# Kernel tuning notes

Measured on AMD Instinct MI355X. Metric: run time of the kernel, lower is better.

## Reference

```python
import jax, jax.numpy as jnp
import numpy as np

B, S, H = 4, 256, 768
E, R, D = 200, 200, 25
NUM_ENT_TYPES, NUM_REL_TYPES = 9, 5
MAX_ENT_LEN = 100


def _make_span_mask(key, b, n, s, max_len):
    k1, k2 = jax.random.split(key)
    start = jax.random.randint(k1, (b, n), 0, s - max_len)
    length = jax.random.randint(k2, (b, n), 1, max_len)
    pos = jnp.arange(s)[None, None, :]
    return ((pos >= start[..., None]) & (pos < (start + length)[..., None])).astype(jnp.int32)


def setup_inputs() -> dict:
    key = jax.random.key(0)
    ks = jax.random.split(key, 9)
    lhs = jax.random.normal(ks[0], (B, S, H), dtype=jnp.float32)
    entity_mask = _make_span_mask(ks[1], B, E, S, 30)          # [B,E,S], span length < MAX_ENT_LEN
    relations = jax.random.randint(ks[2], (B, R, 2), 0, E).astype(jnp.int32)
    relation_context_mask = _make_span_mask(ks[3], B, R, S, 30)  # [B,R,S]
    size_emb = jax.random.normal(ks[4], (MAX_ENT_LEN, D), dtype=jnp.float32) * 0.02
    span_w = jax.random.normal(ks[5], (NUM_ENT_TYPES, D + 2 * H), dtype=jnp.float32) * 0.02
    span_b = jax.random.normal(ks[6], (NUM_ENT_TYPES,), dtype=jnp.float32) * 0.02
    rel_w = jax.random.normal(ks[7], (NUM_REL_TYPES, 2 * D + 3 * H), dtype=jnp.float32) * 0.02
    rel_b = jax.random.normal(ks[8], (NUM_REL_TYPES,), dtype=jnp.float32) * 0.02
    return {"last_hidden_state": lhs, "entity_mask": entity_mask, "relations": relations,
            "relation_context_mask": relation_context_mask, "size_emb": size_emb,
            "span_w": span_w, "span_b": span_b, "rel_w": rel_w, "rel_b": rel_b}


def _masked_maxpool(lhs, mask):
    # lhs: [B,S,H], mask: [B,N,S] (0/1) -> [B,N,H]
    # Faithful to torch: broadcast multiply (zeros included in max), then max over S.
    masked = lhs[:, None, :, :] * mask[:, :, :, None].astype(lhs.dtype)  # [B,N,S,H]
    return masked.max(axis=2)


def reference(last_hidden_state, entity_mask, relations, relation_context_mask,
              size_emb, span_w, span_b, rel_w, rel_b):
    b = last_hidden_state.shape[0]
    # --- entity classification ---
    entity_size = size_emb[entity_mask.sum(axis=-1)]               # [B,E,D]
    entity = _masked_maxpool(last_hidden_state, entity_mask)       # [B,E,H]
    context = last_hidden_state[:, 0, :]                           # CLS pooling [B,H]
    ctx = jnp.broadcast_to(context[:, None, :], entity.shape)      # [B,E,H]
    entity_repr = jnp.concatenate([entity, ctx, entity_size], axis=-1)
    entity_logit = entity_repr @ span_w.T + span_b                 # [B,E,num_entity_types]
    # --- relation classification ---
    rel_ctx = _masked_maxpool(last_hidden_state, relation_context_mask)  # [B,R,H]
    bidx = jnp.arange(b)[:, None, None]
    pair = entity[bidx, relations]                                 # [B,R,2,H]
    pair = pair.reshape(b, relations.shape[1], -1)                 # [B,R,2H]
    pair_size = entity_size[bidx, relations].reshape(b, relations.shape[1], -1)  # [B,R,2D]
    relation_repr = jnp.concatenate([rel_ctx, pair, pair_size], axis=-1)
    relation_logit = relation_repr @ rel_w.T + rel_b               # [B,R,num_relation_types]
    return entity_logit, relation_logit
```

## Files before the change

### kernel.cpp

```cpp
#include <hip/hip_runtime.h>
#include <math.h>

#define Bb 4
#define Ss 256
#define Hh 768
#define Ee 200
#define Rr 200
#define Dd 25
#define NET 9
#define NRT 5
#define ENT_REPR (Dd + 2*Hh)
#define REL_REPR (2*Dd + 3*Hh)
#define TPB 192
#define H4 (Hh/4)
#define NCG 48
#define NLVL 4


__device__ __forceinline__ float4 max4(float4 a, float4 b) {
    return make_float4(fmaxf(a.x, b.x), fmaxf(a.y, b.y),
                       fmaxf(a.z, b.z), fmaxf(a.w, b.w));
}

__global__ __launch_bounds__(256) void rmq_build(
    const float4* __restrict__ lhs4, float4* __restrict__ rmq4)
{
    const int b   = blockIdx.x / NCG;
    const int cg  = blockIdx.x % NCG;
    const int cf0 = cg * 4;
    const int s   = threadIdx.x;

    __shared__ float4 bufA[Ss][5];
    __shared__ float4 bufB[Ss][5];

    const float4* src = lhs4 + ((size_t)b * Ss + s) * H4 + cf0;
    #pragma unroll
    for (int j = 0; j < 4; ++j) bufA[s][j] = src[j];
    __syncthreads();

    float4 (*A)[5] = bufA;
    float4 (*Bf)[5] = bufB;
    #pragma unroll
    for (int l = 1; l <= NLVL; ++l) {
        const int sp = min(s + (1 << (l - 1)), Ss - 1);
        #pragma unroll
        for (int j = 0; j < 4; ++j)
            Bf[s][j] = max4(A[s][j], A[sp][j]);
        __syncthreads();
        float4* lvl = rmq4 + ((size_t)(l - 1) * Bb + b) * Ss * H4 + cf0;
        #pragma unroll
        for (int p = 0; p < 4; ++p) {
            const int sr = (s >> 2) + (p << 6);
            const int j  = s & 3;
            lvl[(size_t)sr * H4 + j] = Bf[sr][j];
        }
        float4 (*t)[5] = A; A = Bf; Bf = t;
        __syncthreads();
    }
}

__device__ __forceinline__ void span_decode(const unsigned long long* bal,
                                            int& first, int& length)
{
    const unsigned long long b0 = bal[0], b1 = bal[1], b2 = bal[2], b3 = bal[3];
    length = __popcll(b0) + __popcll(b1) + __popcll(b2) + __popcll(b3);
    if (b0)      first = __ffsll(b0) - 1;
    else if (b1) first = 63  + __ffsll(b1);
    else if (b2) first = 127 + __ffsll(b2);
    else         first = 191 + __ffsll(b3);
}

__device__ __forceinline__ float4 rmq_query(
    const float4* __restrict__ lhs4, const float4* __restrict__ rmq4,
    int b, int first, int length, int tid)
{
    const int l  = 31 - __clz(length);
    const int i2 = first + length - (1 << l);
    const float4* base = (l == 0)
        ? (lhs4 + (size_t)b * Ss * H4)
        : (rmq4 + ((size_t)(l - 1) * Bb + b) * Ss * H4);
    const float4 t1 = base[(size_t)first * H4 + tid];
    const float4 t2 = base[(size_t)i2    * H4 + tid];
    float4 m = max4(t1, t2);
    return max4(m, make_float4(0.f, 0.f, 0.f, 0.f));
}

__global__ __launch_bounds__(TPB) void spert_fused(
    const float4* __restrict__ lhs4,
    const float4* __restrict__ rmq4,
    const int*   __restrict__ ent_mask,
    const int*   __restrict__ relations,
    const int*   __restrict__ rel_mask,
    const float* __restrict__ size_emb,
    const float* __restrict__ span_w,
    const float* __restrict__ span_b,
    const float* __restrict__ rel_w,
    const float* __restrict__ rel_b,
    float* __restrict__ ent_logit,
    float* __restrict__ rel_logit)
{
    const int tid  = threadIdx.x;
    const int wave = tid >> 6;
    const int lane = tid & 63;

    __shared__ unsigned long long s_bal[3][4];
    __shared__ float s_part[3][NET];

    if (blockIdx.x < Bb * Ee) {
        const int b = blockIdx.x / Ee;
        const int e = blockIdx.x % Ee;

        const int* mrow = ent_mask + (size_t)(b*Ee + e)*Ss;
        {
            const unsigned long long bal = __ballot(mrow[tid] != 0);
            if (lane == 0) s_bal[0][wave] = bal;
        }
        if (tid < 64) {
            const unsigned long long bal = __ballot(mrow[192 + tid] != 0);
            if (tid == 0) s_bal[0][3] = bal;
        }
        __syncthreads();

        int first, length;
        span_decode(s_bal[0], first, length);

        const float4 v  = rmq_query(lhs4, rmq4, b, first, length, tid);
        const float4 cx = lhs4[(size_t)b * Ss * H4 + tid];
        const float  sz = (tid < Dd) ? size_emb[length * Dd + tid] : 0.0f;

        float sums[NET];
        #pragma unroll
        for (int t = 0; t < NET; ++t) {
            const float* w  = span_w + (size_t)t * ENT_REPR;
            const float* wa = w + 4*tid;
            const float* wb = w + Hh + 4*tid;
            float s = v.x*wa[0]  + v.y*wa[1]  + v.z*wa[2]  + v.w*wa[3]
                    + cx.x*wb[0] + cx.y*wb[1] + cx.z*wb[2] + cx.w*wb[3];
            if (tid < Dd) s += sz * w[2*Hh + tid];
            sums[t] = s;
        }
        #pragma unroll
        for (int t = 0; t < NET; ++t) {
            float s = sums[t];
            #pragma unroll
            for (int o = 32; o > 0; o >>= 1) s += __shfl_xor(s, o, 64);
            if (lane == 0) s_part[wave][t] = s;
        }
        __syncthreads();
        if (tid < NET) {
            ent_logit[(size_t)(b*Ee + e)*NET + tid] =
                s_part[0][tid] + s_part[1][tid] + s_part[2][tid] + span_b[tid];
        }
    } else {
        const int idx = blockIdx.x - Bb * Ee;
        const int b = idx / Rr;
        const int r = idx % Rr;

        const int e1 = relations[(size_t)(b*Rr + r)*2 + 0];
        const int e2 = relations[(size_t)(b*Rr + r)*2 + 1];

        const int* mrc = rel_mask + (size_t)(b*Rr + r)*Ss;
        const int* mr1 = ent_mask + (size_t)(b*Ee + e1)*Ss;
        const int* mr2 = ent_mask + (size_t)(b*Ee + e2)*Ss;
        {
            const unsigned long long bc = __ballot(mrc[tid] != 0);
            const unsigned long long b1 = __ballot(mr1[tid] != 0);
            const unsigned long long b2 = __ballot(mr2[tid] != 0);
            if (lane == 0) {
                s_bal[0][wave] = bc;
                s_bal[1][wave] = b1;
                s_bal[2][wave] = b2;
            }
        }
        if (tid < 64) {
            const unsigned long long bc = __ballot(mrc[192 + tid] != 0);
            const unsigned long long b1 = __ballot(mr1[192 + tid] != 0);
            const unsigned long long b2 = __ballot(mr2[192 + tid] != 0);
            if (tid == 0) {
                s_bal[0][3] = bc;
                s_bal[1][3] = b1;
                s_bal[2][3] = b2;
            }
        }
        __syncthreads();

        int fc, nc; span_decode(s_bal[0], fc, nc);
        int f1, n1; span_decode(s_bal[1], f1, n1);
        int f2, n2; span_decode(s_bal[2], f2, n2);

        const float4 cx = rmq_query(lhs4, rmq4, b, fc, nc, tid);
        const float4 a  = rmq_query(lhs4, rmq4, b, f1, n1, tid);
        const float4 d  = rmq_query(lhs4, rmq4, b, f2, n2, tid);
        const float sz1 = (tid < Dd) ? size_emb[n1 * Dd + tid] : 0.0f;
        const float sz2 = (tid < Dd) ? size_emb[n2 * Dd + tid] : 0.0f;

        float sums[NRT];
        #pragma unroll
        for (int t = 0; t < NRT; ++t) {
            const float* w  = rel_w + (size_t)t * REL_REPR;
            const float* wc = w + 4*tid;
            const float* wa = w + Hh + 4*tid;
            const float* wd = w + 2*Hh + 4*tid;
            float s = cx.x*wc[0] + cx.y*wc[1] + cx.z*wc[2] + cx.w*wc[3]
                    + a.x*wa[0]  + a.y*wa[1]  + a.z*wa[2]  + a.w*wa[3]
                    + d.x*wd[0]  + d.y*wd[1]  + d.z*wd[2]  + d.w*wd[3];
            if (tid < Dd) s += sz1 * w[3*Hh + tid] + sz2 * w[3*Hh + Dd + tid];
            sums[t] = s;
        }
        #pragma unroll
        for (int t = 0; t < NRT; ++t) {
            float s = sums[t];
            #pragma unroll
            for (int o = 32; o > 0; o >>= 1) s += __shfl_xor(s, o, 64);
            if (lane == 0) s_part[wave][t] = s;
        }
        __syncthreads();
        if (tid < NRT) {
            rel_logit[(size_t)(b*Rr + r)*NRT + tid] =
                s_part[0][tid] + s_part[1][tid] + s_part[2][tid] + rel_b[tid];
        }
    }
}

extern "C" void kernel_launch(void* const* d_in, const int* in_sizes, int n_in,
                              void* d_out, int out_size, void* d_ws, size_t ws_size,
                              hipStream_t stream) {
    const float* lhs       = (const float*)d_in[0];
    const int*   ent_mask  = (const int*)  d_in[1];
    const int*   relations = (const int*)  d_in[2];
    const int*   rel_mask  = (const int*)  d_in[3];
    const float* size_emb  = (const float*)d_in[4];
    const float* span_w    = (const float*)d_in[5];
    const float* span_b    = (const float*)d_in[6];
    const float* rel_w     = (const float*)d_in[7];
    const float* rel_b     = (const float*)d_in[8];

    float* ent_logit = (float*)d_out;
    float* rel_logit = (float*)d_out + (size_t)Bb*Ee*NET;

    const float4* lhs4 = (const float4*)lhs;
    float4*       rmq4 = (float4*)d_ws;

    rmq_build<<<Bb * NCG, 256, 0, stream>>>(lhs4, rmq4);

    spert_fused<<<Bb*Ee + Bb*Rr, TPB, 0, stream>>>(
        lhs4, rmq4, ent_mask, relations, rel_mask, size_emb,
        span_w, span_b, rel_w, rel_b, ent_logit, rel_logit);
}
```

Before: 85.60 us.

## Map each span/relation to one wavefront and pad weights for float4 loads

Changes the main kernel so each wavefront handles one entity or relation instead of a 192-thread block. Span bounds are decoded with int4 mask loads and wave shuffles, which removes shared memory and block barriers. The weights are copied into a padded workspace in the build kernel so the dot products can use aligned float4 loads. Each lane now does three times the work, and the padding copy adds a small amount of extra work to the build step.

```diff
diff --git a/kernel.cpp b/kernel.cpp
--- a/kernel.cpp
+++ b/kernel.cpp
@@ -9,216 +9,197 @@
 #define Dd 25
 #define NET 9
 #define NRT 5
-#define ENT_REPR (Dd + 2*Hh)
-#define REL_REPR (2*Dd + 3*Hh)
-#define TPB 192
 #define H4 (Hh/4)
 #define NCG 48
 #define NLVL 4
+#define SPAD 1568
+#define RPAD 2368
+#define RMQ_F (4u * Bb * Ss * Hh)
 
 
 __device__ __forceinline__ float4 max4(float4 a, float4 b) {
     return make_float4(fmaxf(a.x, b.x), fmaxf(a.y, b.y),
                        fmaxf(a.z, b.z), fmaxf(a.w, b.w));
 }
-
-__global__ __launch_bounds__(256) void rmq_build(
-    const float4* __restrict__ lhs4, float4* __restrict__ rmq4)
-{
-    const int b   = blockIdx.x / NCG;
-    const int cg  = blockIdx.x % NCG;
-    const int cf0 = cg * 4;
-    const int s   = threadIdx.x;
-
-    __shared__ float4 bufA[Ss][5];
-    __shared__ float4 bufB[Ss][5];
-
-    const float4* src = lhs4 + ((size_t)b * Ss + s) * H4 + cf0;
+__device__ __forceinline__ float dot4(float4 a, float4 b) {
+    return a.x*b.x + a.y*b.y + a.z*b.z + a.w*b.w;
+}
+
+__global__ __launch_bounds__(256) void build_kernel(
+    const float4* __restrict__ lhs4,
+    const float* __restrict__ span_w, const float* __restrict__ rel_w,
+    float4* __restrict__ rmq4,
+    float* __restrict__ span_wp, float* __restrict__ rel_wp)
+{
+    if (blockIdx.x < Bb * NCG) {
+        const int b   = blockIdx.x / NCG;
+        const int cg  = blockIdx.x % NCG;
+        const int cf0 = cg * 4;
+        const int s   = threadIdx.x;
+
+        __shared__ float4 bufA[Ss][5];
+        __shared__ float4 bufB[Ss][5];
+
+        const float4* src = lhs4 + ((size_t)b * Ss + s) * H4 + cf0;
+        #pragma unroll
+        for (int j = 0; j < 4; ++j) bufA[s][j] = src[j];
+        __syncthreads();
+
+        float4 (*A)[5] = bufA;
+        float4 (*Bf)[5] = bufB;
+        #pragma unroll
+        for (int l = 1; l <= NLVL; ++l) {
+            const int sp = min(s + (1 << (l - 1)), Ss - 1);
+            #pragma unroll
+            for (int j = 0; j < 4; ++j)
+                Bf[s][j] = max4(A[s][j], A[sp][j]);
+            __syncthreads();
+            float4* lvl = rmq4 + ((size_t)(l - 1) * Bb + b) * Ss * H4 + cf0;
+            #pragma unroll
+            for (int p = 0; p < 4; ++p) {
+                const int sr = (s >> 2) + (p << 6);
+                const int j  = s & 3;
+                lvl[(size_t)sr * H4 + j] = Bf[sr][j];
+            }
+            float4 (*t)[5] = A; A = Bf; Bf = t;
+            __syncthreads();
+        }
+    } else if (blockIdx.x == Bb * NCG) {
+        for (int i = threadIdx.x; i < NET * SPAD; i += 256) {
+            const int t = i / SPAD, k = i - t * SPAD;
+            span_wp[i] = (k < Dd + 2*Hh) ? span_w[t * (Dd + 2*Hh) + k] : 0.f;
+        }
+    } else {
+        for (int i = threadIdx.x; i < NRT * RPAD; i += 256) {
+            const int t = i / RPAD, k = i - t * RPAD;
+            rel_wp[i] = (k < 2*Dd + 3*Hh) ? rel_w[t * (2*Dd + 3*Hh) + k] : 0.f;
+        }
+    }
+}
+
+__device__ __forceinline__ void span_from_mask(int4 m, int lane,
+                                               int& first, int& length)
+{
+    int cnt = (m.x != 0) + (m.y != 0) + (m.z != 0) + (m.w != 0);
+    const int p = 4 * lane;
+    int fm = 256;
+    if      (m.x) fm = p;
+    else if (m.y) fm = p + 1;
+    else if (m.z) fm = p + 2;
+    else if (m.w) fm = p + 3;
     #pragma unroll
-    for (int j = 0; j < 4; ++j) bufA[s][j] = src[j];
-    __syncthreads();
-
-    float4 (*A)[5] = bufA;
-    float4 (*Bf)[5] = bufB;
-    #pragma unroll
-    for (int l = 1; l <= NLVL; ++l) {
-        const int sp = min(s + (1 << (l - 1)), Ss - 1);
-        #pragma unroll
-        for (int j = 0; j < 4; ++j)
-            Bf[s][j] = max4(A[s][j], A[sp][j]);
-        __syncthreads();
-        float4* lvl = rmq4 + ((size_t)(l - 1) * Bb + b) * Ss * H4 + cf0;
-        #pragma unroll
-        for (int p = 0; p < 4; ++p) {
-            const int sr = (s >> 2) + (p << 6);
-            const int j  = s & 3;
-            lvl[(size_t)sr * H4 + j] = Bf[sr][j];
-        }
-        float4 (*t)[5] = A; A = Bf; Bf = t;
-        __syncthreads();
+    for (int o = 32; o > 0; o >>= 1) {
+        cnt += __shfl_xor(cnt, o, 64);
+        fm   = min(fm, __shfl_xor(fm, o, 64));
     }
-}
-
-__device__ __forceinline__ void span_decode(const unsigned long long* bal,
-                                            int& first, int& length)
-{
-    const unsigned long long b0 = bal[0], b1 = bal[1], b2 = bal[2], b3 = bal[3];
-    length = __popcll(b0) + __popcll(b1) + __popcll(b2) + __popcll(b3);
-    if (b0)      first = __ffsll(b0) - 1;
-    else if (b1) first = 63  + __ffsll(b1);
-    else if (b2) first = 127 + __ffsll(b2);
-    else         first = 191 + __ffsll(b3);
-}
-
-__device__ __forceinline__ float4 rmq_query(
+    first = fm; length = cnt;
+}
+
+__device__ __forceinline__ void rmq_q(
     const float4* __restrict__ lhs4, const float4* __restrict__ rmq4,
-    int b, int first, int length, int tid)
-{
-    const int l  = 31 - __clz(length);
-    const int i2 = first + length - (1 << l);
-    const float4* base = (l == 0)
+    int b, int first, int length, int lane,
+    float4& q0, float4& q1, float4& q2)
+{
+    const int lv = 31 - __clz(length);
+    const int i2 = first + length - (1 << lv);
+    const float4* base = (lv == 0)
         ? (lhs4 + (size_t)b * Ss * H4)
-        : (rmq4 + ((size_t)(l - 1) * Bb + b) * Ss * H4);
-    const float4 t1 = base[(size_t)first * H4 + tid];
-    const float4 t2 = base[(size_t)i2    * H4 + tid];
-    float4 m = max4(t1, t2);
-    return max4(m, make_float4(0.f, 0.f, 0.f, 0.f));
-}
-
-__global__ __launch_bounds__(TPB) void spert_fused(
+        : (rmq4 + ((size_t)(lv - 1) * Bb + b) * Ss * H4);
+    const float4* p1 = base + (size_t)first * H4 + lane;
+    const float4* p2 = base + (size_t)i2    * H4 + lane;
+    const float4 z = make_float4(0.f, 0.f, 0.f, 0.f);
+    q0 = max4(max4(p1[0],   p2[0]),   z);
+    q1 = max4(max4(p1[64],  p2[64]),  z);
+    q2 = max4(max4(p1[128], p2[128]), z);
+}
+
+__global__ __launch_bounds__(256) void spert_fused(
     const float4* __restrict__ lhs4,
     const float4* __restrict__ rmq4,
+    const float* __restrict__ span_wp,
+    const float* __restrict__ rel_wp,
     const int*   __restrict__ ent_mask,
     const int*   __restrict__ relations,
     const int*   __restrict__ rel_mask,
     const float* __restrict__ size_emb,
-    const float* __restrict__ span_w,
     const float* __restrict__ span_b,
-    const float* __restrict__ rel_w,
     const float* __restrict__ rel_b,
     float* __restrict__ ent_logit,
     float* __restrict__ rel_logit)
 {
-    const int tid  = threadIdx.x;
-    const int wave = tid >> 6;
-    const int lane = tid & 63;
-
-    __shared__ unsigned long long s_bal[3][4];
-    __shared__ float s_part[3][NET];
-
-    if (blockIdx.x < Bb * Ee) {
-        const int b = blockIdx.x / Ee;
-        const int e = blockIdx.x % Ee;
-
-        const int* mrow = ent_mask + (size_t)(b*Ee + e)*Ss;
-        {
-            const unsigned long long bal = __ballot(mrow[tid] != 0);
-            if (lane == 0) s_bal[0][wave] = bal;
-        }
-        if (tid < 64) {
-            const unsigned long long bal = __ballot(mrow[192 + tid] != 0);
-            if (tid == 0) s_bal[0][3] = bal;
-        }
-        __syncthreads();
-
+    const int lane = threadIdx.x & 63;
+    const int wid  = blockIdx.x * 4 + (threadIdx.x >> 6);
+
+    if (wid < Bb * Ee) {
+        const int b = wid / Ee;
+        const int e = wid % Ee;
+
+        const int4 m = ((const int4*)(ent_mask + (size_t)(b*Ee + e)*Ss))[lane];
         int first, length;
-        span_decode(s_bal[0], first, length);
-
-        const float4 v  = rmq_query(lhs4, rmq4, b, first, length, tid);
-        const float4 cx = lhs4[(size_t)b * Ss * H4 + tid];
-        const float  sz = (tid < Dd) ? size_emb[length * Dd + tid] : 0.0f;
-
-        float sums[NET];
+        span_from_mask(m, lane, first, length);
+
+        float4 q0, q1, q2;
+        rmq_q(lhs4, rmq4, b, first, length, lane, q0, q1, q2);
+        const float4* lb = lhs4 + (size_t)b * Ss * H4;
+        const float4 c0 = lb[lane], c1 = lb[lane + 64], c2 = lb[lane + 128];
+        const float sz = (lane < Dd) ? size_emb[length * Dd + lane] : 0.0f;
+
+        float outv = 0.0f;
         #pragma unroll
         for (int t = 0; t < NET; ++t) {
-            const float* w  = span_w + (size_t)t * ENT_REPR;
-            const float* wa = w + 4*tid;
-            const float* wb = w + Hh + 4*tid;
-            float s = v.x*wa[0]  + v.y*wa[1]  + v.z*wa[2]  + v.w*wa[3]
-                    + cx.x*wb[0] + cx.y*wb[1] + cx.z*wb[2] + cx.w*wb[3];
-            if (tid < Dd) s += sz * w[2*Hh + tid];
-            sums[t] = s;
-        }
-        #pragma unroll
-        for (int t = 0; t < NET; ++t) {
-            float s = sums[t];
+            const float4* w4 = (const float4*)(span_wp + (size_t)t * SPAD);
+            float s = dot4(q0, w4[lane])        + dot4(q1, w4[lane + 64])
+                    + dot4(q2, w4[lane + 128])
+                    + dot4(c0, w4[192 + lane])  + dot4(c1, w4[256 + lane])
+                    + dot4(c2, w4[320 + lane]);
+            if (lane < Dd) s += sz * span_wp[(size_t)t * SPAD + 2*Hh + lane];
             #pragma unroll
             for (int o = 32; o > 0; o >>= 1) s += __shfl_xor(s, o, 64);
-            if (lane == 0) s_part[wave][t] = s;
-        }
-        __syncthreads();
-        if (tid < NET) {
-            ent_logit[(size_t)(b*Ee + e)*NET + tid] =
-                s_part[0][tid] + s_part[1][tid] + s_part[2][tid] + span_b[tid];
-        }
+            if (lane == t) outv = s + span_b[t];
+        }
+        if (lane < NET) ent_logit[(size_t)(b*Ee + e)*NET + lane] = outv;
     } else {
-        const int idx = blockIdx.x - Bb * Ee;
+        const int idx = wid - Bb * Ee;
         const int b = idx / Rr;
         const int r = idx % Rr;
 
-        const int e1 = relations[(size_t)(b*Rr + r)*2 + 0];
-        const int e2 = relations[(size_t)(b*Rr + r)*2 + 1];
-
-        const int* mrc = rel_mask + (size_t)(b*Rr + r)*Ss;
-        const int* mr1 = ent_mask + (size_t)(b*Ee + e1)*Ss;
-        const int* mr2 = ent_mask + (size_t)(b*Ee + e2)*Ss;
-        {
-            const unsigned long long bc = __ballot(mrc[tid] != 0);
-            const unsigned long long b1 = __ballot(mr1[tid] != 0);
-            const unsigned long long b2 = __ballot(mr2[tid] != 0);
-            if (lane == 0) {
-                s_bal[0][wave] = bc;
-                s_bal[1][wave] = b1;
-                s_bal[2][wave] = b2;
+        const int2 ee = ((const int2*)relations)[(size_t)b*Rr + r];
+        const int e1 = ee.x, e2 = ee.y;
+
+        const int4 mc = ((const int4*)(rel_mask + (size_t)(b*Rr + r)*Ss))[lane];
+        const int4 m1 = ((const int4*)(ent_mask + (size_t)(b*Ee + e1)*Ss))[lane];
+        const int4 m2 = ((const int4*)(ent_mask + (size_t)(b*Ee + e2)*Ss))[lane];
+        int fc, nc, f1, n1, f2, n2;
+        span_from_mask(mc, lane, fc, nc);
+        span_from_mask(m1, lane, f1, n1);
+        span_from_mask(m2, lane, f2, n2);
+
+        float4 x0, x1, x2, a0, a1, a2, d0, d1, d2;
+        rmq_q(lhs4, rmq4, b, fc, nc, lane, x0, x1, x2);
+        rmq_q(lhs4, rmq4, b, f1, n1, lane, a0, a1, a2);
+        rmq_q(lhs4, rmq4, b, f2, n2, lane, d0, d1, d2);
+        const float sz1 = (lane < Dd) ? size_emb[n1 * Dd + lane] : 0.0f;
+        const float sz2 = (lane < Dd) ? size_emb[n2 * Dd + lane] : 0.0f;
+
+        float outv = 0.0f;
+        #pragma unroll
+        for (int t = 0; t < NRT; ++t) {
+            const float4* w4 = (const float4*)(rel_wp + (size_t)t * RPAD);
+            float s = dot4(x0, w4[lane])       + dot4(x1, w4[lane + 64])
+                    + dot4(x2, w4[lane + 128])
+                    + dot4(a0, w4[192 + lane]) + dot4(a1, w4[256 + lane])
+                    + dot4(a2, w4[320 + lane])
+                    + dot4(d0, w4[384 + lane]) + dot4(d1, w4[448 + lane])
+                    + dot4(d2, w4[512 + lane]);
+            if (lane < Dd) {
+                const float* wr = rel_wp + (size_t)t * RPAD + 3*Hh;
+                s += sz1 * wr[lane] + sz2 * wr[Dd + lane];
             }
-        }
-        if (tid < 64) {
-            const unsigned long long bc = __ballot(mrc[192 + tid] != 0);
-            const unsigned long long b1 = __ballot(mr1[192 + tid] != 0);
-            const unsigned long long b2 = __ballot(mr2[192 + tid] != 0);
-            if (tid == 0) {
-                s_bal[0][3] = bc;
-                s_bal[1][3] = b1;
-                s_bal[2][3] = b2;
-            }
-        }
-        __syncthreads();
-
-        int fc, nc; span_decode(s_bal[0], fc, nc);
-        int f1, n1; span_decode(s_bal[1], f1, n1);
-        int f2, n2; span_decode(s_bal[2], f2, n2);
-
-        const float4 cx = rmq_query(lhs4, rmq4, b, fc, nc, tid);
-        const float4 a  = rmq_query(lhs4, rmq4, b, f1, n1, tid);
-        const float4 d  = rmq_query(lhs4, rmq4, b, f2, n2, tid);
-        const float sz1 = (tid < Dd) ? size_emb[n1 * Dd + tid] : 0.0f;
-        const float sz2 = (tid < Dd) ? size_emb[n2 * Dd + tid] : 0.0f;
-
-        float sums[NRT];
-        #pragma unroll
-        for (int t = 0; t < NRT; ++t) {
-            const float* w  = rel_w + (size_t)t * REL_REPR;
-            const float* wc = w + 4*tid;
-            const float* wa = w + Hh + 4*tid;
-            const float* wd = w + 2*Hh + 4*tid;
-            float s = cx.x*wc[0] + cx.y*wc[1] + cx.z*wc[2] + cx.w*wc[3]
-                    + a.x*wa[0]  + a.y*wa[1]  + a.z*wa[2]  + a.w*wa[3]
-                    + d.x*wd[0]  + d.y*wd[1]  + d.z*wd[2]  + d.w*wd[3];
-            if (tid < Dd) s += sz1 * w[3*Hh + tid] + sz2 * w[3*Hh + Dd + tid];
-            sums[t] = s;
-        }
-        #pragma unroll
-        for (int t = 0; t < NRT; ++t) {
-            float s = sums[t];
             #pragma unroll
             for (int o = 32; o > 0; o >>= 1) s += __shfl_xor(s, o, 64);
-            if (lane == 0) s_part[wave][t] = s;
-        }
-        __syncthreads();
-        if (tid < NRT) {
-            rel_logit[(size_t)(b*Rr + r)*NRT + tid] =
-                s_part[0][tid] + s_part[1][tid] + s_part[2][tid] + rel_b[tid];
-        }
+            if (lane == t) outv = s + rel_b[t];
+        }
+        if (lane < NRT) rel_logit[(size_t)(b*Rr + r)*NRT + lane] = outv;
     }
 }
 
@@ -239,11 +220,14 @@
     float* rel_logit = (float*)d_out + (size_t)Bb*Ee*NET;
 
     const float4* lhs4 = (const float4*)lhs;
-    float4*       rmq4 = (float4*)d_ws;
-
-    rmq_build<<<Bb * NCG, 256, 0, stream>>>(lhs4, rmq4);
-
-    spert_fused<<<Bb*Ee + Bb*Rr, TPB, 0, stream>>>(
-        lhs4, rmq4, ent_mask, relations, rel_mask, size_emb,
-        span_w, span_b, rel_w, rel_b, ent_logit, rel_logit);
-}
+    float4* rmq4    = (float4*)d_ws;
+    float*  span_wp = (float*)d_ws + RMQ_F;
+    float*  rel_wp  = span_wp + (size_t)NET * SPAD;
+
+    build_kernel<<<Bb * NCG + 2, 256, 0, stream>>>(
+        lhs4, span_w, rel_w, rmq4, span_wp, rel_wp);
+
+    spert_fused<<<(Bb*Ee + Bb*Rr) / 4, 256, 0, stream>>>(
+        lhs4, rmq4, span_wp, rel_wp, ent_mask, relations, rel_mask,
+        size_emb, span_b, rel_b, ent_logit, rel_logit);
+}
```

Result: slower. 100.3 us (+17.1%).
